# Optimization experiments

Hardware: AMD Instinct MI355X
Metric: run time of the kernel (lower is better)

Reference implementation:

```python
import jax, jax.numpy as jnp
import numpy as np

NEG_SLOPE = 0.01  # PyTorch LeakyReLU default

def lrelu(x):
    return jnp.where(x >= 0, x, NEG_SLOPE * x)

def setup_inputs() -> dict:
    key = jax.random.key(0)
    ks = jax.random.split(key, 16)
    d, nu, ni, nr = 64, 50000, 25000, 400000
    s = 1.0 / np.sqrt(d)
    f = jnp.float32
    return {
        "Xu": jax.random.normal(ks[0], (nu, d), f),
        "Xi": jax.random.normal(ks[1], (ni, d), f),
        "Wsrc": jax.random.normal(ks[2], (d, d), f) * s,
        "bsrc": jnp.zeros((d,), f),
        "Wdst": jax.random.normal(ks[3], (d, d), f) * s,
        "bdst": jnp.zeros((d,), f),
        "watt_rep": jax.random.normal(ks[4], (d,), f) * s,
        "batt_rep": jnp.zeros((), f),
        "Wo": jax.random.normal(ks[5], (d, d), f) * s,
        "bo": jnp.zeros((d,), f),
        "Wu": jax.random.normal(ks[6], (d, d), f) * s,
        "bu": jnp.zeros((d,), f),
        "watt_agg": jax.random.normal(ks[7], (d,), f) * s,
        "batt_agg": jnp.zeros((), f),
        "pref_user": jax.random.normal(ks[8], (nu, d), f),
        "pref_item": jax.random.normal(ks[9], (ni, d), f),
        "r_user": jax.random.randint(ks[10], (400000,), 0, nu),
        "r_item": jax.random.randint(ks[11], (400000,), 0, ni),
    }

def reference(Xu, Xi, Wsrc, bsrc, Wdst, bdst, watt_rep, batt_rep,
              Wo, bo, Wu, bu, watt_agg, batt_agg,
              pref_user, pref_item, r_user, r_item):
    nu, ni = Xu.shape[0], Xi.shape[0]
    # ---- ReviewRepresentationConv ----
    # Each review has exactly one user edge and one item edge, so per-etype
    # mean over edges is a gather; cross-type 'mean' averages the two types.
    agg = 0.5 * (Xu[r_user] + Xi[r_item])                 # [R, d]
    hs_u = Xu @ Wsrc + bsrc                               # src_w_a(x)
    hs_i = Xi @ Wsrc + bsrc
    hd_r = agg @ Wdst + bdst                              # dst_w_a(agg)
    # raw exp attention (module uses torch.exp, not stable edge_softmax here)
    a_u = jnp.exp(lrelu(hs_u[r_user] + hd_r) @ watt_rep + batt_rep)  # [R]
    a_i = jnp.exp(lrelu(hs_i[r_item] + hd_r) @ watt_rep + batt_rep)
    denom = a_u + a_i                                     # e_div_v normalizer
    h_rev = (a_u / denom)[:, None] * Xu[r_user] + (a_i / denom)[:, None] * Xi[r_item]
    # ---- ReviewAggregatorConv ----
    h_o = h_rev @ Wo + bo                                 # w_o(src review feats)

    def agg_side(npid_emb, dst, n_dst):
        z = lrelu(h_o + npid_emb @ Wu + bu)               # u_add_e then LeakyReLU
        a = z @ watt_agg + batt_agg                       # [R] attention logits
        m = jax.ops.segment_max(a, dst, num_segments=n_dst)
        e = jnp.exp(a - m[dst])                           # stable edge_softmax
        ssum = jax.ops.segment_sum(e, dst, num_segments=n_dst)
        w = e / ssum[dst]
        # u_mul_e + sum scatter-reduce
        return jax.ops.segment_sum(h_rev * w[:, None], dst, num_segments=n_dst)

    out_user = agg_side(pref_item[r_item], r_user, nu)    # [nu, d]
    out_item = agg_side(pref_user[r_user], r_item, ni)    # [ni, d]
    return jnp.concatenate([out_user, out_item], axis=0)  # [nu+ni, d]
```

## Files before the change

### kernel.cpp

```cpp
#include <hip/hip_runtime.h>
#include <hip/hip_fp16.h>
#include <math.h>

#define D 64
#define EPB 1024

struct __align__(8) h4 { __half2 a; __half2 b; };

typedef _Float16 f16x8 __attribute__((ext_vector_type(8)));
typedef float f32x4 __attribute__((ext_vector_type(4)));

__device__ __forceinline__ float lrelu(float x) { return fmaxf(x, 0.f) + 0.01f * fminf(x, 0.f); }
__device__ __forceinline__ __half2 u2h(unsigned v) { union { unsigned u; __half2 h; } c; c.u = v; return c.h; }

__global__ void k_count(const int* __restrict__ ru, const int* __restrict__ ri,
                        int* __restrict__ cnt_u, int* __restrict__ cnt_i, int R) {
    int r = blockIdx.x * blockDim.x + threadIdx.x;
    if (r >= R) return;
    atomicAdd(&cnt_u[ru[r]], 1);
    atomicAdd(&cnt_i[ri[r]], 1);
}

__global__ void k_fill_u(const int* __restrict__ ru, const int* __restrict__ ri,
                         int* __restrict__ cur_u, int2* __restrict__ edges, int R) {
    int r = blockIdx.x * blockDim.x + threadIdx.x;
    if (r >= R) return;
    int u = ru[r], it = ri[r];
    int j = atomicAdd(&cur_u[u], 1);
    edges[j] = make_int2(u, it);
}

__global__ __launch_bounds__(256) void k_nodes_mfma(
    const float* __restrict__ Xu, const float* __restrict__ Pu, int nu, int ntu,
    const float* __restrict__ Xi_, const float* __restrict__ Pi, int ni, int nti,
    const float* __restrict__ Wsrc, const float* __restrict__ bsrc,
    const float* __restrict__ Wdst, const float* __restrict__ bdst,
    const float* __restrict__ Wo,   const float* __restrict__ bo,
    const float* __restrict__ Wu,   const float* __restrict__ bu,
    h4* __restrict__ packU, __half* __restrict__ Xuh,
    h4* __restrict__ packI, __half* __restrict__ Xih) {
    __shared__ __half sD[4][16][72];
    __shared__ float sb[4][64];
    int tid = threadIdx.x;
    int lane = tid & 63, w = tid >> 6;
    int col = lane & 15, kg = lane >> 4;

    {
        int c = tid & 63, m = tid >> 6;
        const float* bp = (m == 0) ? bsrc : (m == 1) ? bdst : (m == 2) ? bo : bu;
        sb[m][c] = bp[c];
    }
    const float* W = (w == 0) ? Wsrc : (w == 1) ? Wdst : (w == 2) ? Wo : Wu;
    f16x8 Bf[2][4];
#pragma unroll
    for (int kt = 0; kt < 2; ++kt)
#pragma unroll
        for (int ct = 0; ct < 4; ++ct) {
            int c = ct * 16 + col;
            int k0 = kt * 32 + kg * 8;
            f16x8 b;
#pragma unroll
            for (int j = 0; j < 8; ++j) b[j] = (_Float16)W[(k0 + j) * 64 + c];
            Bf[kt][ct] = b;
        }
    __syncthreads();

    int T = ntu + nti;
    for (int tile = blockIdx.x; tile < T; tile += gridDim.x) {
        bool usr = tile < ntu;
        const float* X = usr ? Xu : Xi_;
        const float* P = usr ? Pu : Pi;
        h4* pack = usr ? packU : packI;
        __half* Xh = usr ? Xuh : Xih;
        int n = usr ? nu : ni;
        int nb = (usr ? tile : tile - ntu) * 16;

        int arow = nb + col; if (arow >= n) arow = n - 1;
        const float* src = (w == 3) ? P : X;
        const float4* rp0 = (const float4*)(src + (size_t)arow * 64 + kg * 8);
        const float4* rp1 = (const float4*)(src + (size_t)arow * 64 + 32 + kg * 8);
        float4 a0 = rp0[0], a1 = rp0[1];
        float4 a2 = rp1[0], a3 = rp1[1];
        f16x8 A0, A1;
        A0[0] = (_Float16)a0.x; A0[1] = (_Float16)a0.y; A0[2] = (_Float16)a0.z; A0[3] = (_Float16)a0.w;
        A0[4] = (_Float16)a1.x; A0[5] = (_Float16)a1.y; A0[6] = (_Float16)a1.z; A0[7] = (_Float16)a1.w;
        A1[0] = (_Float16)a2.x; A1[1] = (_Float16)a2.y; A1[2] = (_Float16)a2.z; A1[3] = (_Float16)a2.w;
        A1[4] = (_Float16)a3.x; A1[5] = (_Float16)a3.y; A1[6] = (_Float16)a3.z; A1[7] = (_Float16)a3.w;
        if (w == 0) {
            *(f16x8*)(Xh + (size_t)arow * 64 + kg * 8) = A0;
            *(f16x8*)(Xh + (size_t)arow * 64 + 32 + kg * 8) = A1;
        }
        f32x4 acc[4];
#pragma unroll
        for (int ct = 0; ct < 4; ++ct) {
            acc[ct] = (f32x4){0.f, 0.f, 0.f, 0.f};
            acc[ct] = __builtin_amdgcn_mfma_f32_16x16x32_f16(A0, Bf[0][ct], acc[ct], 0, 0, 0);
            acc[ct] = __builtin_amdgcn_mfma_f32_16x16x32_f16(A1, Bf[1][ct], acc[ct], 0, 0, 0);
        }
        __syncthreads();
#pragma unroll
        for (int ct = 0; ct < 4; ++ct)
#pragma unroll
            for (int jj = 0; jj < 4; ++jj)
                sD[w][kg * 4 + jj][ct * 16 + col] = __float2half(acc[ct][jj]);
        __syncthreads();
        int r = tid >> 4, c0 = (tid & 15) * 4;
        int node = nb + r;
        if (node < n) {
            __align__(16) h4 out[4];
#pragma unroll
            for (int q = 0; q < 4; ++q) {
                int c = c0 + q;
                float hs = __half2float(sD[0][r][c]) + sb[0][c];
                float hds = 0.5f * (__half2float(sD[1][r][c]) + sb[1][c]);
                float f0 = hs + hds;
                float ho = __half2float(sD[2][r][c]) + sb[2][c];
                float pw = __half2float(sD[3][r][c]) + sb[3][c];
                out[q].a = __floats2half2_rn(f0, hds);
                out[q].b = __floats2half2_rn(ho, pw);
            }
            uint4* dst = (uint4*)(pack + (size_t)node * 64 + c0);
            dst[0] = *(uint4*)&out[0];
            dst[1] = *(uint4*)&out[2];
        }
    }
}

__global__ __launch_bounds__(256, 1) void k_rev1(
    const int2* __restrict__ edges,
    const float4* __restrict__ packU4, const float4* __restrict__ packI4,
    const float4* __restrict__ watt_rep4,
    const float4* __restrict__ watt_agg4, const float* __restrict__ batt_agg,
    int* __restrict__ cur_i,
    float4* __restrict__ pay_su, float4* __restrict__ pay_si,
    int R) {
    int tid = threadIdx.x;
    int lane = tid & 63;
    int g16 = lane >> 4;
    int f = lane & 15;
    int j = blockIdx.x * 16 + (tid >> 6) * 4 + g16;
    if (j >= R) return;
    int2 e = edges[j];
    int u = e.x, it = e.y;
    size_t bu_ = (size_t)u * 32 + 2 * f;
    size_t bi_ = (size_t)it * 32 + 2 * f;
    float4 U0 = packU4[bu_], U1 = packU4[bu_ + 1];
    float4 I0 = packI4[bi_], I1 = packI4[bi_ + 1];
    unsigned u0x = __float_as_uint(U0.x), u0y = __float_as_uint(U0.y);
    unsigned u0z = __float_as_uint(U0.z), u0w = __float_as_uint(U0.w);
    unsigned u1x = __float_as_uint(U1.x), u1y = __float_as_uint(U1.y);
    unsigned u1z = __float_as_uint(U1.z), u1w = __float_as_uint(U1.w);
    unsigned i0x = __float_as_uint(I0.x), i0y = __float_as_uint(I0.y);
    unsigned i0z = __float_as_uint(I0.z), i0w = __float_as_uint(I0.w);
    unsigned i1x = __float_as_uint(I1.x), i1y = __float_as_uint(I1.y);
    unsigned i1z = __float_as_uint(I1.z), i1w = __float_as_uint(I1.w);
    __half2 f0u_a = u2h((u0x & 0xFFFFu) | (u0z << 16)), f0u_b = u2h((u1x & 0xFFFFu) | (u1z << 16));
    __half2 hdu_a = u2h((u0x >> 16) | (u0z & 0xFFFF0000u)), hdu_b = u2h((u1x >> 16) | (u1z & 0xFFFF0000u));
    __half2 hou_a = u2h((u0y & 0xFFFFu) | (u0w << 16)), hou_b = u2h((u1y & 0xFFFFu) | (u1w << 16));
    __half2 pwu_a = u2h((u0y >> 16) | (u0w & 0xFFFF0000u)), pwu_b = u2h((u1y >> 16) | (u1w & 0xFFFF0000u));
    __half2 f0i_a = u2h((i0x & 0xFFFFu) | (i0z << 16)), f0i_b = u2h((i1x & 0xFFFFu) | (i1z << 16));
    __half2 hdi_a = u2h((i0x >> 16) | (i0z & 0xFFFF0000u)), hdi_b = u2h((i1x >> 16) | (i1z & 0xFFFF0000u));
    __half2 hoi_a = u2h((i0y & 0xFFFFu) | (i0w << 16)), hoi_b = u2h((i1y & 0xFFFFu) | (i1w << 16));
    __half2 pwi_a = u2h((i0y >> 16) | (i0w & 0xFFFF0000u)), pwi_b = u2h((i1y >> 16) | (i1w & 0xFFFF0000u));

    float2 xu_a = __half22float2(__hadd2(f0u_a, hdi_a)), xu_b = __half22float2(__hadd2(f0u_b, hdi_b));
    float2 xi_a = __half22float2(__hadd2(f0i_a, hdu_a)), xi_b = __half22float2(__hadd2(f0i_b, hdu_b));
    float4 wr = watt_rep4[f];
    float tu = lrelu(xu_a.x) * wr.x + lrelu(xu_a.y) * wr.y + lrelu(xu_b.x) * wr.z + lrelu(xu_b.y) * wr.w;
    float ti = lrelu(xi_a.x) * wr.x + lrelu(xi_a.y) * wr.y + lrelu(xi_b.x) * wr.z + lrelu(xi_b.y) * wr.w;
#pragma unroll
    for (int o = 8; o; o >>= 1) {
        tu += __shfl_xor(tu, o, 64);
        ti += __shfl_xor(ti, o, 64);
    }
    float wu = 1.f / (1.f + __expf(ti - tu));
    __half2 wu2 = __float2half2_rn(wu);
    __half2 wi2 = __float2half2_rn(1.f - wu);
    __half2 ho_a = __hfma2(wu2, hou_a, __hmul2(wi2, hoi_a));
    __half2 ho_b = __hfma2(wu2, hou_b, __hmul2(wi2, hoi_b));
    float2 su_a = __half22float2(__hadd2(ho_a, pwi_a)), su_b = __half22float2(__hadd2(ho_b, pwi_b));
    float2 si_a = __half22float2(__hadd2(ho_a, pwu_a)), si_b = __half22float2(__hadd2(ho_b, pwu_b));
    float4 wa = watt_agg4[f];
    float zu = lrelu(su_a.x) * wa.x + lrelu(su_a.y) * wa.y + lrelu(su_b.x) * wa.z + lrelu(su_b.y) * wa.w;
    float zi = lrelu(si_a.x) * wa.x + lrelu(si_a.y) * wa.y + lrelu(si_b.x) * wa.z + lrelu(si_b.y) * wa.w;
#pragma unroll
    for (int o = 8; o; o >>= 1) {
        zu += __shfl_xor(zu, o, 64);
        zi += __shfl_xor(zi, o, 64);
    }
    if (f == 0) {
        float ba = batt_agg[0];
        pay_su[j] = make_float4(zu + ba, wu, __int_as_float(it), 0.f);
        int j2 = atomicAdd(&cur_i[it], 1);
        pay_si[j2] = make_float4(zi + ba, wu, __int_as_float(u), 0.f);
    }
}

__global__ __launch_bounds__(256) void k_scan_local(
    const int* __restrict__ cnt_u, int* __restrict__ off_u, int nu,
    const int* __restrict__ cnt_i, int* __restrict__ off_i, int ni,
    int* __restrict__ bsum, int Bu) {
    int b = blockIdx.x;
    const int* cnt; int* off; int n; int lb;
    if (b < Bu) { cnt = cnt_u; off = off_u; n = nu; lb = b; }
    else        { cnt = cnt_i; off = off_i; n = ni; lb = b - Bu; }
    int t = threadIdx.x;
    int idx0 = lb * EPB + t * 4;
    int v[4];
#pragma unroll
    for (int k = 0; k < 4; ++k) v[k] = (idx0 + k < n) ? cnt[idx0 + k] : 0;
    int s = v[0] + v[1] + v[2] + v[3];
    int lane = t & 63, w = t >> 6;
    int x = s;
#pragma unroll
    for (int o = 1; o < 64; o <<= 1) {
        int y = __shfl_up(x, o, 64);
        if (lane >= o) x += y;
    }
    __shared__ int wsum[4];
    if (lane == 63) wsum[w] = x;
    __syncthreads();
    int woff = 0;
    for (int j = 0; j < w; ++j) woff += wsum[j];
    int run = woff + x - s;
#pragma unroll
    for (int k = 0; k < 4; ++k) {
        if (idx0 + k < n) off[idx0 + k] = run;
        run += v[k];
    }
    if (t == 255) bsum[b] = woff + x;
}

__global__ __launch_bounds__(256) void k_scan_add(
    int* __restrict__ off_u, int* __restrict__ cur_u, int nu,
    int* __restrict__ off_i, int* __restrict__ cur_i, int ni,
    const int* __restrict__ bsum, int Bu, int Bi) {
    int b = blockIdx.x;
    int* off; int* cur; int n; int lb; const int* bs; int B;
    if (b < Bu) { off = off_u; cur = cur_u; n = nu; lb = b; bs = bsum; B = Bu; }
    else        { off = off_i; cur = cur_i; n = ni; lb = b - Bu; bs = bsum + Bu; B = Bi; }
    int boff = 0;
    for (int j = 0; j < lb; ++j) boff += bs[j];
    int idx0 = lb * EPB + threadIdx.x * 4;
#pragma unroll
    for (int k = 0; k < 4; ++k) {
        int idx = idx0 + k;
        if (idx < n) {
            int vv = off[idx] + boff;
            off[idx] = vv;
            cur[idx] = vv;
        }
    }
    if (lb == B - 1 && threadIdx.x == 0) off[n] = boff + bs[lb];
}

__global__ __launch_bounds__(256, 1) void k_agg(
    const int* __restrict__ off_u, const int* __restrict__ off_i,
    const float4* __restrict__ pay_su, const float4* __restrict__ pay_si,
    const float* __restrict__ Xu, const float* __restrict__ Xi,
    const __half* __restrict__ Xuh, const __half* __restrict__ Xih,
    float* __restrict__ out, int nu, int ntot) {
    int tid = threadIdx.x;
    int lane = tid & 63;
    int idx = blockIdx.x * 4 + (tid >> 6);
    if (idx >= ntot) return;
    bool user = idx < nu;
    int d = user ? idx : idx - nu;
    const int*    offp = user ? off_u : off_i;
    const float4* pay  = user ? pay_su : pay_si;
    const float*  Xown = user ? Xu : Xi;
    const __half* Xoth = user ? Xih : Xuh;
    int s = offp[d], e = offp[d + 1];
    if (s == e) { out[(size_t)idx * D + lane] = 0.f; return; }
    int g = lane >> 3;
    int l = lane & 7;
    float msum = 0.f, mcoef = 0.f;
    float acc[8] = {0.f, 0.f, 0.f, 0.f, 0.f, 0.f, 0.f, 0.f};
    for (int j = s + g; j < e; j += 8) {
        float4 p = pay[j];
        float ex = __expf(p.x);
        float wown = user ? p.y : 1.f - p.y;
        msum += ex;
        mcoef += ex * wown;
        float cv = ex * (1.f - wown);
        int o2 = __float_as_int(p.z);
        const __half2* row = (const __half2*)(Xoth + (size_t)o2 * D + 8 * l);
        float2 f0 = __half22float2(row[0]);
        float2 f1 = __half22float2(row[1]);
        float2 f2 = __half22float2(row[2]);
        float2 f3 = __half22float2(row[3]);
        acc[0] += cv * f0.x; acc[1] += cv * f0.y;
        acc[2] += cv * f1.x; acc[3] += cv * f1.y;
        acc[4] += cv * f2.x; acc[5] += cv * f2.y;
        acc[6] += cv * f3.x; acc[7] += cv * f3.y;
    }
#pragma unroll
    for (int o = 32; o >= 8; o >>= 1) {
        msum  += __shfl_xor(msum, o, 64);
        mcoef += __shfl_xor(mcoef, o, 64);
#pragma unroll
        for (int q = 0; q < 8; ++q) acc[q] += __shfl_xor(acc[q], o, 64);
    }
    if (g == 0) {
        float inv = 1.f / msum;
        const float4* xo = (const float4*)(Xown + (size_t)d * D + 8 * l);
        float4 x0 = xo[0], x1 = xo[1];
        float4 r0, r1;
        r0.x = (mcoef * x0.x + acc[0]) * inv;
        r0.y = (mcoef * x0.y + acc[1]) * inv;
        r0.z = (mcoef * x0.z + acc[2]) * inv;
        r0.w = (mcoef * x0.w + acc[3]) * inv;
        r1.x = (mcoef * x1.x + acc[4]) * inv;
        r1.y = (mcoef * x1.y + acc[5]) * inv;
        r1.z = (mcoef * x1.z + acc[6]) * inv;
        r1.w = (mcoef * x1.w + acc[7]) * inv;
        float4* op = (float4*)(out + (size_t)idx * D + 8 * l);
        op[0] = r0;
        op[1] = r1;
    }
}

extern "C" void kernel_launch(void* const* d_in, const int* in_sizes, int n_in,
                              void* d_out, int out_size, void* d_ws, size_t ws_size,
                              hipStream_t stream) {
    const float* Xu        = (const float*)d_in[0];
    const float* Xi        = (const float*)d_in[1];
    const float* Wsrc      = (const float*)d_in[2];
    const float* bsrc      = (const float*)d_in[3];
    const float* Wdst      = (const float*)d_in[4];
    const float* bdst      = (const float*)d_in[5];
    const float* watt_rep  = (const float*)d_in[6];
    const float* batt_rep  = (const float*)d_in[7];  (void)batt_rep;
    const float* Wo        = (const float*)d_in[8];
    const float* bo        = (const float*)d_in[9];
    const float* Wu        = (const float*)d_in[10];
    const float* bu        = (const float*)d_in[11];
    const float* watt_agg  = (const float*)d_in[12];
    const float* batt_agg  = (const float*)d_in[13];
    const float* pref_user = (const float*)d_in[14];
    const float* pref_item = (const float*)d_in[15];
    const int* r_user      = (const int*)d_in[16];
    const int* r_item      = (const int*)d_in[17];

    int nu = in_sizes[0] / D;
    int ni = in_sizes[1] / D;
    int R  = in_sizes[16];

    float* ws = (float*)d_ws;
    size_t off = 0;
    h4* packU = (h4*)(ws + off); off += (size_t)nu * D * 2;
    h4* packI = (h4*)(ws + off); off += (size_t)ni * D * 2;
    __half* Xuh = (__half*)(ws + off); off += (size_t)nu * D / 2;
    __half* Xih = (__half*)(ws + off); off += (size_t)ni * D / 2;
    float4* pay_su = (float4*)(ws + off); off += (size_t)R * 4;
    float4* pay_si = (float4*)(ws + off); off += (size_t)R * 4;
    int2* edges = (int2*)(ws + off); off += (size_t)R * 2;
    int* cnt_u = (int*)(ws + off); off += (size_t)nu;
    int* cnt_i = (int*)(ws + off); off += (size_t)ni;
    int* bsum  = (int*)(ws + off); off += 256;
    int* off_u = (int*)(ws + off); off += (size_t)nu + 1;
    int* off_i = (int*)(ws + off); off += (size_t)ni + 1;

    hipMemsetAsync(cnt_u, 0, (size_t)(nu + ni) * sizeof(int), stream);

    k_count<<<(R + 255) / 256, 256, 0, stream>>>(r_user, r_item, cnt_u, cnt_i, R);

    int Bu = (nu + EPB - 1) / EPB, Bi = (ni + EPB - 1) / EPB;
    k_scan_local<<<Bu + Bi, 256, 0, stream>>>(
        cnt_u, off_u, nu, cnt_i, off_i, ni, bsum, Bu);
    k_scan_add<<<Bu + Bi, 256, 0, stream>>>(
        off_u, cnt_u, nu, off_i, cnt_i, ni, bsum, Bu, Bi);

    k_fill_u<<<(R + 255) / 256, 256, 0, stream>>>(r_user, r_item, cnt_u, edges, R);

    int ntu = (nu + 15) / 16, nti = (ni + 15) / 16;
    k_nodes_mfma<<<1024, 256, 0, stream>>>(
        Xu, pref_user, nu, ntu, Xi, pref_item, ni, nti,
        Wsrc, bsrc, Wdst, bdst, Wo, bo, Wu, bu,
        packU, Xuh, packI, Xih);

    k_rev1<<<(R + 15) / 16, 256, 0, stream>>>(
        edges, (const float4*)packU, (const float4*)packI,
        (const float4*)watt_rep, (const float4*)watt_agg, batt_agg,
        cnt_i, pay_su, pay_si, R);

    int ntot = nu + ni;
    k_agg<<<(ntot + 3) / 4, 256, 0, stream>>>(
        off_u, off_i, pay_su, pay_si,
        Xu, Xi, Xuh, Xih, (float*)d_out, nu, ntot);
}
```

Baseline: 169.2 us.

## Store node pack as planar fp16 arrays and process each review with 8 lanes

The per-node packed buffer changes from interleaved half2 quadruples to four contiguous 64-wide fp16 planes per node, written with f16x4 stores. The review kernel now reads each plane as 16-byte f16x8 vectors, so it no longer needs the bit-shuffle unpacking. Each review is handled by 8 lanes instead of 16, with shorter shuffle reductions, and twice as many reviews go to each block. More of the math now runs in fp32, so each lane does more work and holds more registers.

```diff
diff --git a/kernel.cpp b/kernel.cpp
--- a/kernel.cpp
+++ b/kernel.cpp
@@ -5,13 +5,11 @@
 #define D 64
 #define EPB 1024
 
-struct __align__(8) h4 { __half2 a; __half2 b; };
-
 typedef _Float16 f16x8 __attribute__((ext_vector_type(8)));
+typedef _Float16 f16x4 __attribute__((ext_vector_type(4)));
 typedef float f32x4 __attribute__((ext_vector_type(4)));
 
 __device__ __forceinline__ float lrelu(float x) { return fmaxf(x, 0.f) + 0.01f * fminf(x, 0.f); }
-__device__ __forceinline__ __half2 u2h(unsigned v) { union { unsigned u; __half2 h; } c; c.u = v; return c.h; }
 
 __global__ void k_count(const int* __restrict__ ru, const int* __restrict__ ri,
                         int* __restrict__ cnt_u, int* __restrict__ cnt_i, int R) {
@@ -37,8 +35,8 @@
     const float* __restrict__ Wdst, const float* __restrict__ bdst,
     const float* __restrict__ Wo,   const float* __restrict__ bo,
     const float* __restrict__ Wu,   const float* __restrict__ bu,
-    h4* __restrict__ packU, __half* __restrict__ Xuh,
-    h4* __restrict__ packI, __half* __restrict__ Xih) {
+    __half* __restrict__ packU, __half* __restrict__ Xuh,
+    __half* __restrict__ packI, __half* __restrict__ Xih) {
     __shared__ __half sD[4][16][72];
     __shared__ float sb[4][64];
     int tid = threadIdx.x;
@@ -70,7 +68,7 @@
         bool usr = tile < ntu;
         const float* X = usr ? Xu : Xi_;
         const float* P = usr ? Pu : Pi;
-        h4* pack = usr ? packU : packI;
+        __half* pack = usr ? packU : packI;
         __half* Xh = usr ? Xuh : Xih;
         int n = usr ? nu : ni;
         int nb = (usr ? tile : tile - ntu) * 16;
@@ -107,28 +105,30 @@
         int r = tid >> 4, c0 = (tid & 15) * 4;
         int node = nb + r;
         if (node < n) {
-            __align__(16) h4 out[4];
+            __half* dst = pack + (size_t)node * 256;
+            f16x4 v[4];
 #pragma unroll
             for (int q = 0; q < 4; ++q) {
                 int c = c0 + q;
                 float hs = __half2float(sD[0][r][c]) + sb[0][c];
                 float hds = 0.5f * (__half2float(sD[1][r][c]) + sb[1][c]);
-                float f0 = hs + hds;
                 float ho = __half2float(sD[2][r][c]) + sb[2][c];
                 float pw = __half2float(sD[3][r][c]) + sb[3][c];
-                out[q].a = __floats2half2_rn(f0, hds);
-                out[q].b = __floats2half2_rn(ho, pw);
+                v[0][q] = (_Float16)(hs + hds);
+                v[1][q] = (_Float16)hds;
+                v[2][q] = (_Float16)ho;
+                v[3][q] = (_Float16)pw;
             }
-            uint4* dst = (uint4*)(pack + (size_t)node * 64 + c0);
-            dst[0] = *(uint4*)&out[0];
-            dst[1] = *(uint4*)&out[2];
+#pragma unroll
+            for (int m = 0; m < 4; ++m)
+                *(f16x4*)(dst + m * 64 + c0) = v[m];
         }
     }
 }
 
 __global__ __launch_bounds__(256, 1) void k_rev1(
     const int2* __restrict__ edges,
-    const float4* __restrict__ packU4, const float4* __restrict__ packI4,
+    const __half* __restrict__ packU, const __half* __restrict__ packI,
     const float4* __restrict__ watt_rep4,
     const float4* __restrict__ watt_agg4, const float* __restrict__ batt_agg,
     int* __restrict__ cur_i,
@@ -136,63 +136,60 @@
     int R) {
     int tid = threadIdx.x;
     int lane = tid & 63;
-    int g16 = lane >> 4;
-    int f = lane & 15;
-    int j = blockIdx.x * 16 + (tid >> 6) * 4 + g16;
+    int f = lane & 7;
+    int j = blockIdx.x * 32 + (tid >> 6) * 8 + (lane >> 3);
     if (j >= R) return;
     int2 e = edges[j];
-    int u = e.x, it = e.y;
-    size_t bu_ = (size_t)u * 32 + 2 * f;
-    size_t bi_ = (size_t)it * 32 + 2 * f;
-    float4 U0 = packU4[bu_], U1 = packU4[bu_ + 1];
-    float4 I0 = packI4[bi_], I1 = packI4[bi_ + 1];
-    unsigned u0x = __float_as_uint(U0.x), u0y = __float_as_uint(U0.y);
-    unsigned u0z = __float_as_uint(U0.z), u0w = __float_as_uint(U0.w);
-    unsigned u1x = __float_as_uint(U1.x), u1y = __float_as_uint(U1.y);
-    unsigned u1z = __float_as_uint(U1.z), u1w = __float_as_uint(U1.w);
-    unsigned i0x = __float_as_uint(I0.x), i0y = __float_as_uint(I0.y);
-    unsigned i0z = __float_as_uint(I0.z), i0w = __float_as_uint(I0.w);
-    unsigned i1x = __float_as_uint(I1.x), i1y = __float_as_uint(I1.y);
-    unsigned i1z = __float_as_uint(I1.z), i1w = __float_as_uint(I1.w);
-    __half2 f0u_a = u2h((u0x & 0xFFFFu) | (u0z << 16)), f0u_b = u2h((u1x & 0xFFFFu) | (u1z << 16));
-    __half2 hdu_a = u2h((u0x >> 16) | (u0z & 0xFFFF0000u)), hdu_b = u2h((u1x >> 16) | (u1z & 0xFFFF0000u));
-    __half2 hou_a = u2h((u0y & 0xFFFFu) | (u0w << 16)), hou_b = u2h((u1y & 0xFFFFu) | (u1w << 16));
-    __half2 pwu_a = u2h((u0y >> 16) | (u0w & 0xFFFF0000u)), pwu_b = u2h((u1y >> 16) | (u1w & 0xFFFF0000u));
-    __half2 f0i_a = u2h((i0x & 0xFFFFu) | (i0z << 16)), f0i_b = u2h((i1x & 0xFFFFu) | (i1z << 16));
-    __half2 hdi_a = u2h((i0x >> 16) | (i0z & 0xFFFF0000u)), hdi_b = u2h((i1x >> 16) | (i1z & 0xFFFF0000u));
-    __half2 hoi_a = u2h((i0y & 0xFFFFu) | (i0w << 16)), hoi_b = u2h((i1y & 0xFFFFu) | (i1w << 16));
-    __half2 pwi_a = u2h((i0y >> 16) | (i0w & 0xFFFF0000u)), pwi_b = u2h((i1y >> 16) | (i1w & 0xFFFF0000u));
-
-    float2 xu_a = __half22float2(__hadd2(f0u_a, hdi_a)), xu_b = __half22float2(__hadd2(f0u_b, hdi_b));
-    float2 xi_a = __half22float2(__hadd2(f0i_a, hdu_a)), xi_b = __half22float2(__hadd2(f0i_b, hdu_b));
-    float4 wr = watt_rep4[f];
-    float tu = lrelu(xu_a.x) * wr.x + lrelu(xu_a.y) * wr.y + lrelu(xu_b.x) * wr.z + lrelu(xu_b.y) * wr.w;
-    float ti = lrelu(xi_a.x) * wr.x + lrelu(xi_a.y) * wr.y + lrelu(xi_b.x) * wr.z + lrelu(xi_b.y) * wr.w;
-#pragma unroll
-    for (int o = 8; o; o >>= 1) {
+    const __half* pu = packU + (size_t)e.x * 256 + f * 8;
+    const __half* pi = packI + (size_t)e.y * 256 + f * 8;
+    f16x8 f0u = *(const f16x8*)(pu);
+    f16x8 hdu = *(const f16x8*)(pu + 64);
+    f16x8 hou = *(const f16x8*)(pu + 128);
+    f16x8 pwu = *(const f16x8*)(pu + 192);
+    f16x8 f0i = *(const f16x8*)(pi);
+    f16x8 hdi = *(const f16x8*)(pi + 64);
+    f16x8 hoi = *(const f16x8*)(pi + 128);
+    f16x8 pwi = *(const f16x8*)(pi + 192);
+
+    f16x8 xu = f0u + hdi;
+    f16x8 xi = f0i + hdu;
+    float4 wrA = watt_rep4[f * 2], wrB = watt_rep4[f * 2 + 1];
+    float tu =
+        lrelu((float)xu[0]) * wrA.x + lrelu((float)xu[1]) * wrA.y +
+        lrelu((float)xu[2]) * wrA.z + lrelu((float)xu[3]) * wrA.w +
+        lrelu((float)xu[4]) * wrB.x + lrelu((float)xu[5]) * wrB.y +
+        lrelu((float)xu[6]) * wrB.z + lrelu((float)xu[7]) * wrB.w;
+    float ti =
+        lrelu((float)xi[0]) * wrA.x + lrelu((float)xi[1]) * wrA.y +
+        lrelu((float)xi[2]) * wrA.z + lrelu((float)xi[3]) * wrA.w +
+        lrelu((float)xi[4]) * wrB.x + lrelu((float)xi[5]) * wrB.y +
+        lrelu((float)xi[6]) * wrB.z + lrelu((float)xi[7]) * wrB.w;
+#pragma unroll
+    for (int o = 4; o; o >>= 1) {
         tu += __shfl_xor(tu, o, 64);
         ti += __shfl_xor(ti, o, 64);
     }
     float wu = 1.f / (1.f + __expf(ti - tu));
-    __half2 wu2 = __float2half2_rn(wu);
-    __half2 wi2 = __float2half2_rn(1.f - wu);
-    __half2 ho_a = __hfma2(wu2, hou_a, __hmul2(wi2, hoi_a));
-    __half2 ho_b = __hfma2(wu2, hou_b, __hmul2(wi2, hoi_b));
-    float2 su_a = __half22float2(__hadd2(ho_a, pwi_a)), su_b = __half22float2(__hadd2(ho_b, pwi_b));
-    float2 si_a = __half22float2(__hadd2(ho_a, pwu_a)), si_b = __half22float2(__hadd2(ho_b, pwu_b));
-    float4 wa = watt_agg4[f];
-    float zu = lrelu(su_a.x) * wa.x + lrelu(su_a.y) * wa.y + lrelu(su_b.x) * wa.z + lrelu(su_b.y) * wa.w;
-    float zi = lrelu(si_a.x) * wa.x + lrelu(si_a.y) * wa.y + lrelu(si_b.x) * wa.z + lrelu(si_b.y) * wa.w;
-#pragma unroll
-    for (int o = 8; o; o >>= 1) {
+    float wi = 1.f - wu;
+    float4 waA = watt_agg4[f * 2], waB = watt_agg4[f * 2 + 1];
+    float zu = 0.f, zi = 0.f;
+#pragma unroll
+    for (int k = 0; k < 8; ++k) {
+        float ho = wu * (float)hou[k] + wi * (float)hoi[k];
+        float wa = (k < 4) ? ((const float*)&waA)[k] : ((const float*)&waB)[k - 4];
+        zu += lrelu(ho + (float)pwi[k]) * wa;
+        zi += lrelu(ho + (float)pwu[k]) * wa;
+    }
+#pragma unroll
+    for (int o = 4; o; o >>= 1) {
         zu += __shfl_xor(zu, o, 64);
         zi += __shfl_xor(zi, o, 64);
     }
     if (f == 0) {
         float ba = batt_agg[0];
-        pay_su[j] = make_float4(zu + ba, wu, __int_as_float(it), 0.f);
-        int j2 = atomicAdd(&cur_i[it], 1);
-        pay_si[j2] = make_float4(zi + ba, wu, __int_as_float(u), 0.f);
+        pay_su[j] = make_float4(zu + ba, wu, __int_as_float(e.y), 0.f);
+        int j2 = atomicAdd(&cur_i[e.y], 1);
+        pay_si[j2] = make_float4(zi + ba, wu, __int_as_float(e.x), 0.f);
     }
 }
 
@@ -348,8 +345,8 @@
 
     float* ws = (float*)d_ws;
     size_t off = 0;
-    h4* packU = (h4*)(ws + off); off += (size_t)nu * D * 2;
-    h4* packI = (h4*)(ws + off); off += (size_t)ni * D * 2;
+    __half* packU = (__half*)(ws + off); off += (size_t)nu * D * 2;
+    __half* packI = (__half*)(ws + off); off += (size_t)ni * D * 2;
     __half* Xuh = (__half*)(ws + off); off += (size_t)nu * D / 2;
     __half* Xih = (__half*)(ws + off); off += (size_t)ni * D / 2;
     float4* pay_su = (float4*)(ws + off); off += (size_t)R * 4;
@@ -379,8 +376,8 @@
         Wsrc, bsrc, Wdst, bdst, Wo, bo, Wu, bu,
         packU, Xuh, packI, Xih);
 
-    k_rev1<<<(R + 15) / 16, 256, 0, stream>>>(
-        edges, (const float4*)packU, (const float4*)packI,
+    k_rev1<<<(R + 31) / 32, 256, 0, stream>>>(
+        edges, packU, packI,
         (const float4*)watt_rep, (const float4*)watt_agg, batt_agg,
         cnt_i, pay_su, pay_si, R);
 
```

New measurement: 165.9 us. About the same (-2.0%).
